# Performance work log

Hardware: AMD Instinct MI355X
Metric: run time of the kernel (lower is better)

## Reference

```python
import jax, jax.numpy as jnp
import numpy as np

S, N, A = 64, 4096, 32
HID, DM, NH, DK = 256, 128, 4, 32
EPS = 1e-5
SCALE = float(np.sqrt(DK))


def setup_inputs() -> dict:
    key = jax.random.key(0)
    ks = jax.random.split(key, 20)
    w = lambda i, sh: jax.random.normal(ks[i], sh, jnp.float32) * 0.02
    z = lambda n: jnp.zeros((n,), jnp.float32)
    return {
        "agent_states": jax.random.normal(ks[0], (N, S), jnp.float32),
        "sw1": w(1, (N * S, HID)), "sb1": z(HID),
        "sw2": w(2, (HID, HID)), "sb2": z(HID),
        "sow": w(3, (HID, 64)), "sob": z(64),
        "tw": w(4, (S + 64, DM)), "tb": z(DM),
        "wq": w(5, (DM, DM)), "bq": z(DM),
        "wk": w(6, (DM, DM)), "bk": z(DM),
        "wv": w(7, (DM, DM)), "bv": z(DM),
        "wo": w(8, (DM, DM)), "bo": z(DM),
        "ln_g": jnp.ones((DM,), jnp.float32), "ln_b": z(DM),
        "taw1": w(9, (DM, 64)), "tab1": z(64),
        "taw2": w(10, (64, 32)), "tab2": z(32),
        "ow1": w(11, (S + DM + 32, 256)), "ob1": z(256),
        "ow2": w(12, (256, DM)), "ob2": z(DM),
        "aw": w(13, (DM, A)), "ab": z(A),
        "vw": w(14, (DM, 1)), "vb": z(1),
        "cw": w(15, (S, 64)), "cb": z(64),
        "cdw": w(16, (64, 32)), "cdb": z(32),
    }


def reference(agent_states, sw1, sb1, sw2, sb2, sow, sob, tw, tb,
              wq, bq, wk, bk, wv, bv, wo, bo, ln_g, ln_b,
              taw1, tab1, taw2, tab2, ow1, ob1, ow2, ob2,
              aw, ab, vw, vb, cw, cb, cdw, cdb):
    n = agent_states.shape[0]
    # strategic level: flatten all agent states -> global objective [64]
    gs = agent_states.reshape(-1)
    strat = jax.nn.relu(jax.nn.relu(gs @ sw1 + sb1) @ sw2 + sb2)
    gobj = strat @ sow + sob
    # tactical encode (batched over agents instead of Python loop)
    tact_in = jnp.concatenate(
        [agent_states, jnp.broadcast_to(gobj, (n, gobj.shape[0]))], axis=-1)
    tact = jax.nn.relu(tact_in @ tw + tb)[None]  # [1, n, DM]
    # multi-head attention across agents
    q = (tact @ wq + bq).reshape(1, n, NH, DK).transpose(0, 2, 1, 3)
    k = (tact @ wk + bk).reshape(1, n, NH, DK).transpose(0, 2, 1, 3)
    v = (tact @ wv + bv).reshape(1, n, NH, DK).transpose(0, 2, 1, 3)
    scores = jnp.einsum('bhqd,bhkd->bhqk', q, k) / SCALE
    attn = jax.nn.softmax(scores, axis=-1)  # [1, NH, n, n]
    ctx = jnp.einsum('bhqk,bhkd->bhqd', attn, v).transpose(0, 2, 1, 3).reshape(1, n, DM)
    res = ctx @ wo + bo + tact
    mu = res.mean(-1, keepdims=True)
    var = res.var(-1, keepdims=True)  # biased, like torch LayerNorm
    coord = ((res - mu) / jnp.sqrt(var + EPS) * ln_g + ln_b)[0]  # [n, DM]
    # task allocation (softmax over 32 tasks)
    task = jax.nn.softmax(jax.nn.relu(coord @ taw1 + tab1) @ taw2 + tab2, axis=-1)
    # operational level -> actions / values
    op_in = jnp.concatenate([agent_states, coord, task], axis=-1)
    opf = jax.nn.relu(jax.nn.relu(op_in @ ow1 + ob1) @ ow2 + ob2)
    actions = opf @ aw + ab
    values = opf @ vw + vb
    # communication messages (two stacked linears, no activation in source)
    messages = (agent_states @ cw + cb) @ cdw + cdb
    return actions, values, messages, task, attn, gobj
```

## Files before the change

kernel.cpp:

```cpp
#include <hip/hip_runtime.h>

typedef __attribute__((ext_vector_type(8))) short s8v;
typedef __attribute__((ext_vector_type(4))) float f4v;

#define MFMA16(a, b, c) __builtin_amdgcn_mfma_f32_16x16x32_bf16((a), (b), (c), 0, 0, 0)

#define NAG   4096
#define SDIM  64
#define DMOD  128
#define NHD   4
#define DKD   32
#define HIDD  256
static constexpr float INV_SCALE = 0.17677669529663687f;
static constexpr float EPSV = 1e-5f;

#define OFF_ACT   0
#define OFF_VAL   131072
#define OFF_MSG   135168
#define OFF_TASK  266240
#define OFF_ATTN  397312
#define OFF_GOBJ  67506176

static constexpr size_t WS_P1   = 0;
static constexpr size_t WS_P1B  = 524288;
static constexpr size_t WS_P2   = 540672;
static constexpr size_t WS_TACT = 558080;
static constexpr size_t WS_Q    = 2655232;
static constexpr size_t WS_K    = 3703808;
static constexpr size_t WS_VT   = 4752384;
static constexpr size_t WS_CTX  = 5800960;
static constexpr size_t WS_OPIN = 7898112;
static constexpr size_t WS_H    = 9733120;
static constexpr size_t WS_OPF  = 11830272;
static constexpr size_t WS_OW1T = 12878848;
static constexpr size_t WS_OW2T = 12993536;

typedef unsigned short u16;
typedef unsigned int   u32;

static __device__ __forceinline__ u16 f2bf(float f) {
    union { float f; u32 u; } x; x.f = f;
    u32 r = x.u + 0x7FFFu + ((x.u >> 16) & 1u);
    return (u16)(r >> 16);
}
static __device__ __forceinline__ float bf2f(u16 b) {
    union { u32 u; float f; } x; x.u = ((u32)b) << 16;
    return x.f;
}

__global__ __launch_bounds__(256) void k1_sw1(const float* __restrict__ gs,
                                              const float* __restrict__ sw1,
                                              float* __restrict__ p1,
                                              const float* __restrict__ ow1,
                                              const float* __restrict__ ow2,
                                              u16* __restrict__ w1t,
                                              u16* __restrict__ w2t) {
    int tid = threadIdx.x;
    int b = blockIdx.x;
    if (b >= 512) {
        int bb = b - 512;
        if (bb < 224) {
            w1t[tid * 224 + bb] = f2bf(ow1[bb * 256 + tid]);
        } else if (tid < 128) {
            int k0 = (bb - 224) * 8;
#pragma unroll
            for (int kk = 0; kk < 8; ++kk) {
                int k = k0 + kk;
                w2t[tid * 256 + k] = f2bf(ow2[k * 128 + tid]);
            }
        }
        return;
    }
    __shared__ float gsl[512];
    __shared__ float red[4][256];
    gsl[tid]       = gs[b * 512 + tid];
    gsl[tid + 256] = gs[b * 512 + 256 + tid];
    __syncthreads();
    int t = tid & 63;
    int rg = tid >> 6;
    const f4v* w4 = (const f4v*)sw1;
    f4v acc = {0.f, 0.f, 0.f, 0.f};
    size_t rb = (size_t)b * 512;
#pragma unroll 4
    for (int r = rg; r < 512; r += 4) {
        float g = gsl[r];
        f4v w = __builtin_nontemporal_load(&w4[(rb + r) * 64 + t]);
        acc[0] += g * w[0]; acc[1] += g * w[1]; acc[2] += g * w[2]; acc[3] += g * w[3];
    }
    red[rg][4 * t + 0] = acc[0]; red[rg][4 * t + 1] = acc[1];
    red[rg][4 * t + 2] = acc[2]; red[rg][4 * t + 3] = acc[3];
    __syncthreads();
    float s = red[0][tid] + red[1][tid] + red[2][tid] + red[3][tid];
    p1[b * 256 + tid] = s;
}

__global__ void k1b_red(const float* __restrict__ p1, float* __restrict__ p1b) {
    int j = threadIdx.x;
    int b0 = blockIdx.x * 32;
    float s = 0.f;
#pragma unroll
    for (int b = 0; b < 32; ++b) s += p1[(b0 + b) * 256 + j];
    p1b[blockIdx.x * 256 + j] = s;
}

__global__ void k2b_strat(const float* __restrict__ p1b, const float* __restrict__ sb1,
                          const float* __restrict__ sw2, float* __restrict__ p2) {
    __shared__ float h1[256];
    int j = threadIdx.x;
    float s = 0.f;
#pragma unroll
    for (int b = 0; b < 16; ++b) s += p1b[b * 256 + j];
    h1[j] = fmaxf(s + sb1[j], 0.f);
    __syncthreads();
    int i0 = blockIdx.x * 16;
    float acc = 0.f;
#pragma unroll
    for (int i = 0; i < 16; ++i) acc += h1[i0 + i] * sw2[(i0 + i) * 256 + j];
    p2[blockIdx.x * 256 + j] = acc;
}

__global__ __launch_bounds__(256) void k3_tact_qkv(
    const float* __restrict__ p2, const float* __restrict__ sb2,
    const float* __restrict__ sow, const float* __restrict__ sob,
    const float* __restrict__ as, const float* __restrict__ tw, const float* __restrict__ tb,
    const float* __restrict__ wq, const float* __restrict__ bq,
    const float* __restrict__ wk, const float* __restrict__ bk,
    const float* __restrict__ wv, const float* __restrict__ bv,
    float* __restrict__ out_gobj, float* __restrict__ tactws,
    u16* __restrict__ qws, u16* __restrict__ kws, u16* __restrict__ vtws) {
    __shared__ float strat[256];
    __shared__ float gobj[64];
    __shared__ float asl[16][64];
    __shared__ float tl[16][128];
    int tid = threadIdx.x;
    int a0 = blockIdx.x * 16;
    {
        float s = 0.f;
#pragma unroll
        for (int b = 0; b < 16; ++b) s += p2[b * 256 + tid];
        strat[tid] = fmaxf(s + sb2[tid], 0.f);
    }
#pragma unroll
    for (int r = 0; r < 4; ++r) {
        int idx = tid + r * 256;
        asl[idx >> 6][idx & 63] = as[a0 * 64 + idx];
    }
    __syncthreads();
    if (tid < 64) {
        float g = sob[tid];
        for (int i = 0; i < 256; ++i) g += strat[i] * sow[i * 64 + tid];
        gobj[tid] = g;
        if (blockIdx.x == 0) out_gobj[tid] = g;
    }
    __syncthreads();
    int ah = tid >> 7, j = tid & 127;
    float gacc = 0.f;
    for (int i = 0; i < 64; ++i) gacc += gobj[i] * tw[(64 + i) * 128 + j];
    float acc[8];
    float base = tb[j] + gacc;
#pragma unroll
    for (int a = 0; a < 8; ++a) acc[a] = base;
    for (int i = 0; i < 64; ++i) {
        float w = tw[i * 128 + j];
#pragma unroll
        for (int a = 0; a < 8; ++a) acc[a] += asl[ah * 8 + a][i] * w;
    }
#pragma unroll
    for (int a = 0; a < 8; ++a) {
        float t = fmaxf(acc[a], 0.f);
        tl[ah * 8 + a][j] = t;
        tactws[(size_t)(a0 + ah * 8 + a) * 128 + j] = t;
    }
    __syncthreads();
    int h = j >> 5, d = j & 31;
#pragma unroll
    for (int a = 0; a < 8; ++a) acc[a] = 0.f;
    for (int i = 0; i < 128; ++i) {
        float w = wq[i * 128 + j];
#pragma unroll
        for (int a = 0; a < 8; ++a) acc[a] += tl[ah * 8 + a][i] * w;
    }
#pragma unroll
    for (int a = 0; a < 8; ++a)
        qws[h * 131072 + (a0 + ah * 8 + a) * 32 + d] = f2bf((acc[a] + bq[j]) * INV_SCALE);
#pragma unroll
    for (int a = 0; a < 8; ++a) acc[a] = 0.f;
    for (int i = 0; i < 128; ++i) {
        float w = wk[i * 128 + j];
#pragma unroll
        for (int a = 0; a < 8; ++a) acc[a] += tl[ah * 8 + a][i] * w;
    }
#pragma unroll
    for (int a = 0; a < 8; ++a)
        kws[h * 131072 + (a0 + ah * 8 + a) * 32 + d] = f2bf(acc[a] + bk[j]);
#pragma unroll
    for (int a = 0; a < 8; ++a) acc[a] = 0.f;
    for (int i = 0; i < 128; ++i) {
        float w = wv[i * 128 + j];
#pragma unroll
        for (int a = 0; a < 8; ++a) acc[a] += tl[ah * 8 + a][i] * w;
    }
    union { u16 u[8]; s8v v; } pk;
#pragma unroll
    for (int a = 0; a < 8; ++a) pk.u[a] = f2bf(acc[a] + bv[j]);
    *(s8v*)(vtws + h * 131072 + d * 4096 + a0 + ah * 8) = pk.v;
}

__global__ __launch_bounds__(512) void k4_attn(
    const u16* __restrict__ qws, const u16* __restrict__ kws, const u16* __restrict__ vtws,
    float* __restrict__ attn, float* __restrict__ ctxws) {
    int tid = threadIdx.x;
    int wid = tid >> 6;
    int l = tid & 63;
    int g = l >> 4;
    int ln = l & 15;
    int h = blockIdx.x >> 8;
    int qt = (blockIdx.x & 255) * 16;
    const u16* qh = qws + h * 131072;
    const u16* kh = kws + h * 131072;
    const u16* vh = vtws + h * 131072;
    int j0 = wid * 512;

    s8v aq = *(const s8v*)(qh + (qt + ln) * 32 + 8 * g);
    f4v zero = {0.f, 0.f, 0.f, 0.f};

    __shared__ __align__(16) union SmemU {
        struct {
            float red[8][16];
            u16 ldsPb[8][2][16][40];
            float pctx[8][16][32];
        } a;
        float sT[16][516];
    } sm;

    f4v lacc = zero, accA = zero, accB = zero;
    int buf = 0;
    for (int jc = 0; jc < 16; ++jc) {
        int jb = j0 + jc * 32;
        s8v b0 = *(const s8v*)(kh + (jb + ln) * 32 + 8 * g);
        s8v b1 = *(const s8v*)(kh + (jb + 16 + ln) * 32 + 8 * g);
        f4v S0 = MFMA16(aq, b0, zero);
        f4v S1 = MFMA16(aq, b1, zero);
#pragma unroll
        for (int r = 0; r < 4; ++r) {
            float w0 = __expf(S0[r]);
            float w1 = __expf(S1[r]);
            lacc[r] += w0 + w1;
            sm.a.ldsPb[wid][buf][4 * g + r][ln] = f2bf(w0);
            sm.a.ldsPb[wid][buf][4 * g + r][16 + ln] = f2bf(w1);
        }
        s8v bp = *(const s8v*)&sm.a.ldsPb[wid][buf][ln][8 * g];
        s8v va = *(const s8v*)(vh + ln * 4096 + jb + 8 * g);
        s8v vb = *(const s8v*)(vh + (16 + ln) * 4096 + jb + 8 * g);
        accA = MFMA16(va, bp, accA);
        accB = MFMA16(vb, bp, accB);
        buf ^= 1;
    }
#pragma unroll
    for (int m = 1; m <= 8; m <<= 1) {
        lacc[0] += __shfl_xor(lacc[0], m);
        lacc[1] += __shfl_xor(lacc[1], m);
        lacc[2] += __shfl_xor(lacc[2], m);
        lacc[3] += __shfl_xor(lacc[3], m);
    }
    if (ln == 0) {
#pragma unroll
        for (int r = 0; r < 4; ++r) sm.a.red[wid][4 * g + r] = lacc[r];
    }
    __syncthreads();
    float linvq = 1.f / (sm.a.red[0][ln] + sm.a.red[1][ln] + sm.a.red[2][ln] + sm.a.red[3][ln] +
                         sm.a.red[4][ln] + sm.a.red[5][ln] + sm.a.red[6][ln] + sm.a.red[7][ln]);
#pragma unroll
    for (int r = 0; r < 4; ++r) {
        sm.a.pctx[wid][ln][4 * g + r] = accA[r] * linvq;
        sm.a.pctx[wid][ln][16 + 4 * g + r] = accB[r] * linvq;
    }
    __syncthreads();
    {
        int q = tid >> 5;
        int d = tid & 31;
        float s = sm.a.pctx[0][q][d] + sm.a.pctx[1][q][d] + sm.a.pctx[2][q][d] + sm.a.pctx[3][q][d] +
                  sm.a.pctx[4][q][d] + sm.a.pctx[5][q][d] + sm.a.pctx[6][q][d] + sm.a.pctx[7][q][d];
        ctxws[(size_t)(qt + q) * 128 + h * 32 + d] = s;
    }
    __syncthreads();

    float* attnh = attn + (size_t)h * 4096 * 4096;
    for (int c = 0; c < 8; ++c) {
#pragma unroll
        for (int it = 0; it < 2; ++it) {
            int co = wid * 64 + it * 32;
            int jb = c * 512 + co;
            s8v b0 = *(const s8v*)(kh + (jb + ln) * 32 + 8 * g);
            s8v b1 = *(const s8v*)(kh + (jb + 16 + ln) * 32 + 8 * g);
            f4v S0 = MFMA16(b0, aq, zero);
            f4v S1 = MFMA16(b1, aq, zero);
            f4v o0, o1;
#pragma unroll
            for (int r = 0; r < 4; ++r) {
                o0[r] = __expf(S0[r]) * linvq;
                o1[r] = __expf(S1[r]) * linvq;
            }
            *(f4v*)&sm.sT[ln][co + 4 * g] = o0;
            *(f4v*)&sm.sT[ln][co + 16 + 4 * g] = o1;
        }
        __syncthreads();
#pragma unroll
        for (int r2 = 0; r2 < 2; ++r2) {
            int row = 2 * wid + r2;
            float* dst = attnh + (size_t)(qt + row) * 4096 + c * 512;
            f4v t0 = *(const f4v*)&sm.sT[row][4 * l];
            f4v t1 = *(const f4v*)&sm.sT[row][256 + 4 * l];
            *(f4v*)(dst + 4 * l) = t0;
            *(f4v*)(dst + 256 + 4 * l) = t1;
        }
        __syncthreads();
    }
}

__global__ __launch_bounds__(512) void k5_post(
    const float* __restrict__ ctxws, const float* __restrict__ tactws,
    const float* __restrict__ wo, const float* __restrict__ bo,
    const float* __restrict__ lng, const float* __restrict__ lnb,
    const float* __restrict__ taw1, const float* __restrict__ tab1,
    const float* __restrict__ taw2, const float* __restrict__ tab2,
    const float* __restrict__ as, float* __restrict__ dout, u16* __restrict__ opin) {
    __shared__ float wos[128 * 128];
    __shared__ float tw1s[128 * 64];
    __shared__ float tw2s[64 * 32];
    __shared__ float cx[8][128];
    __shared__ float coords[8][128];
    __shared__ float t1v[8][64];
    int tid = threadIdx.x;
    for (int i = tid; i < 128 * 128; i += 512) wos[i] = wo[i];
    for (int i = tid; i < 128 * 64; i += 512) tw1s[i] = taw1[i];
    for (int i = tid; i < 64 * 32; i += 512) tw2s[i] = taw2[i];
    __syncthreads();
    int w = tid >> 6, l = tid & 63;
    for (int it = 0; it < 2; ++it) {
        int n = blockIdx.x * 16 + w * 2 + it;
        float c0 = ctxws[(size_t)n * 128 + l], c1 = ctxws[(size_t)n * 128 + 64 + l];
        float t0 = tactws[(size_t)n * 128 + l], t1 = tactws[(size_t)n * 128 + 64 + l];
        float av = as[n * 64 + l];
        cx[w][l] = c0; cx[w][64 + l] = c1;
        __syncthreads();
        float r0 = bo[l] + t0, r1 = bo[64 + l] + t1;
        for (int k = 0; k < 128; ++k) {
            float cv = cx[w][k];
            r0 += cv * wos[k * 128 + l];
            r1 += cv * wos[k * 128 + 64 + l];
        }
        float s = r0 + r1;
#pragma unroll
        for (int m = 1; m <= 32; m <<= 1) s += __shfl_xor(s, m);
        float mu = s * (1.f / 128.f);
        float d0 = r0 - mu, d1 = r1 - mu;
        float vs = d0 * d0 + d1 * d1;
#pragma unroll
        for (int m = 1; m <= 32; m <<= 1) vs += __shfl_xor(vs, m);
        float rstd = 1.f / sqrtf(vs * (1.f / 128.f) + EPSV);
        float co0 = d0 * rstd * lng[l] + lnb[l];
        float co1 = d1 * rstd * lng[64 + l] + lnb[64 + l];
        coords[w][l] = co0; coords[w][64 + l] = co1;
        opin[(size_t)n * 224 + l] = f2bf(av);
        opin[(size_t)n * 224 + 64 + l] = f2bf(co0);
        opin[(size_t)n * 224 + 128 + l] = f2bf(co1);
        __syncthreads();
        float a1 = tab1[l];
        for (int i = 0; i < 128; ++i) a1 += coords[w][i] * tw1s[i * 64 + l];
        t1v[w][l] = fmaxf(a1, 0.f);
        __syncthreads();
        if (l < 32) {
            float a2 = tab2[l];
            for (int i = 0; i < 64; ++i) a2 += t1v[w][i] * tw2s[i * 32 + l];
            float mx = a2;
#pragma unroll
            for (int m = 1; m <= 16; m <<= 1) mx = fmaxf(mx, __shfl_xor(mx, m));
            float e = __expf(a2 - mx);
            float se = e;
#pragma unroll
            for (int m = 1; m <= 16; m <<= 1) se += __shfl_xor(se, m);
            float tk = e / se;
            dout[OFF_TASK + n * 32 + l] = tk;
            opin[(size_t)n * 224 + 192 + l] = f2bf(tk);
        }
        __syncthreads();
    }
}

__global__ __launch_bounds__(256) void k6a(const u16* __restrict__ opin, const u16* __restrict__ w1t,
                                           const float* __restrict__ ob1, u16* __restrict__ Hws) {
    int tid = threadIdx.x;
    int w = tid >> 6, l = tid & 63, g = l >> 4, ln = l & 15;
    int bm = blockIdx.x & 63, bn = blockIdx.x >> 6;
    int m0 = bm * 64 + w * 16, n0 = bn * 64;
    f4v acc[4];
    f4v zero = {0.f, 0.f, 0.f, 0.f};
#pragma unroll
    for (int nt = 0; nt < 4; ++nt) acc[nt] = zero;
    for (int kt = 0; kt < 7; ++kt) {
        s8v A = *(const s8v*)(opin + (size_t)(m0 + ln) * 224 + kt * 32 + 8 * g);
#pragma unroll
        for (int nt = 0; nt < 4; ++nt) {
            s8v B = *(const s8v*)(w1t + (size_t)(n0 + nt * 16 + ln) * 224 + kt * 32 + 8 * g);
            acc[nt] = MFMA16(A, B, acc[nt]);
        }
    }
#pragma unroll
    for (int nt = 0; nt < 4; ++nt) {
        int col = n0 + nt * 16 + ln;
        float bias = ob1[col];
#pragma unroll
        for (int r = 0; r < 4; ++r) {
            int row = m0 + 4 * g + r;
            Hws[(size_t)row * 256 + col] = f2bf(fmaxf(acc[nt][r] + bias, 0.f));
        }
    }
}

__global__ __launch_bounds__(256) void k6b(const u16* __restrict__ Hws, const u16* __restrict__ w2t,
                                           const float* __restrict__ ob2, u16* __restrict__ opfws) {
    int tid = threadIdx.x;
    int w = tid >> 6, l = tid & 63, g = l >> 4, ln = l & 15;
    int bm = blockIdx.x & 63, bn = blockIdx.x >> 6;
    int m0 = bm * 64 + w * 16, n0 = bn * 64;
    f4v acc[4];
    f4v zero = {0.f, 0.f, 0.f, 0.f};
#pragma unroll
    for (int nt = 0; nt < 4; ++nt) acc[nt] = zero;
    for (int kt = 0; kt < 8; ++kt) {
        s8v A = *(const s8v*)(Hws + (size_t)(m0 + ln) * 256 + kt * 32 + 8 * g);
#pragma unroll
        for (int nt = 0; nt < 4; ++nt) {
            s8v B = *(const s8v*)(w2t + (size_t)(n0 + nt * 16 + ln) * 256 + kt * 32 + 8 * g);
            acc[nt] = MFMA16(A, B, acc[nt]);
        }
    }
#pragma unroll
    for (int nt = 0; nt < 4; ++nt) {
        int col = n0 + nt * 16 + ln;
        float bias = ob2[col];
#pragma unroll
        for (int r = 0; r < 4; ++r) {
            int row = m0 + 4 * g + r;
            opfws[(size_t)row * 128 + col] = f2bf(fmaxf(acc[nt][r] + bias, 0.f));
        }
    }
}

__global__ __launch_bounds__(256) void k6c(const u16* __restrict__ opf, const float* __restrict__ as,
                                           const float* __restrict__ aw, const float* __restrict__ ab,
                                           const float* __restrict__ vw, const float* __restrict__ vb,
                                           const float* __restrict__ cw, const float* __restrict__ cb,
                                           const float* __restrict__ cdw, const float* __restrict__ cdb,
                                           float* __restrict__ dout) {
    __shared__ float opfs[4][128];
    __shared__ float asl[4][64];
    __shared__ float m1s[4][64];
    int tid = threadIdx.x;
    int w = tid >> 6, l = tid & 63;
    int n = blockIdx.x * 4 + w;
    {
        u32 u = *(const u32*)(opf + (size_t)n * 128 + 2 * l);
        opfs[w][2 * l] = bf2f((u16)(u & 0xffff));
        opfs[w][2 * l + 1] = bf2f((u16)(u >> 16));
        asl[w][l] = as[n * 64 + l];
    }
    __syncthreads();
    if (l < 32) {
        float a = ab[l];
        for (int k = 0; k < 128; ++k) a += opfs[w][k] * aw[k * 32 + l];
        dout[OFF_ACT + n * 32 + l] = a;
    }
    {
        float p = opfs[w][l] * vw[l] + opfs[w][64 + l] * vw[64 + l];
#pragma unroll
        for (int m = 1; m <= 32; m <<= 1) p += __shfl_xor(p, m);
        if (l == 0) dout[OFF_VAL + n] = p + vb[0];
    }
    {
        float a = cb[l];
        for (int k = 0; k < 64; ++k) a += asl[w][k] * cw[k * 64 + l];
        m1s[w][l] = a;
    }
    __syncthreads();
    if (l < 32) {
        float a = cdb[l];
        for (int k = 0; k < 64; ++k) a += m1s[w][k] * cdw[k * 32 + l];
        dout[OFF_MSG + n * 32 + l] = a;
    }
}

extern "C" void kernel_launch(void* const* d_in, const int* in_sizes, int n_in,
                              void* d_out, int out_size, void* d_ws, size_t ws_size,
                              hipStream_t stream) {
    const float* as  = (const float*)d_in[0];
    const float* sw1 = (const float*)d_in[1];
    const float* sb1 = (const float*)d_in[2];
    const float* sw2 = (const float*)d_in[3];
    const float* sb2 = (const float*)d_in[4];
    const float* sow = (const float*)d_in[5];
    const float* sob = (const float*)d_in[6];
    const float* tw  = (const float*)d_in[7];
    const float* tb  = (const float*)d_in[8];
    const float* wq  = (const float*)d_in[9];
    const float* bq  = (const float*)d_in[10];
    const float* wk  = (const float*)d_in[11];
    const float* bk  = (const float*)d_in[12];
    const float* wv  = (const float*)d_in[13];
    const float* bv  = (const float*)d_in[14];
    const float* wo  = (const float*)d_in[15];
    const float* bo  = (const float*)d_in[16];
    const float* lng = (const float*)d_in[17];
    const float* lnb = (const float*)d_in[18];
    const float* taw1 = (const float*)d_in[19];
    const float* tab1 = (const float*)d_in[20];
    const float* taw2 = (const float*)d_in[21];
    const float* tab2 = (const float*)d_in[22];
    const float* ow1 = (const float*)d_in[23];
    const float* ob1 = (const float*)d_in[24];
    const float* ow2 = (const float*)d_in[25];
    const float* ob2 = (const float*)d_in[26];
    const float* aw  = (const float*)d_in[27];
    const float* ab  = (const float*)d_in[28];
    const float* vw  = (const float*)d_in[29];
    const float* vb  = (const float*)d_in[30];
    const float* cw  = (const float*)d_in[31];
    const float* cb  = (const float*)d_in[32];
    const float* cdw = (const float*)d_in[33];
    const float* cdb = (const float*)d_in[34];

    float* dout = (float*)d_out;
    char* ws = (char*)d_ws;
    float* p1    = (float*)(ws + WS_P1);
    float* p1b   = (float*)(ws + WS_P1B);
    float* p2    = (float*)(ws + WS_P2);
    float* tactw = (float*)(ws + WS_TACT);
    u16*   qws   = (u16*)(ws + WS_Q);
    u16*   kws   = (u16*)(ws + WS_K);
    u16*   vtws  = (u16*)(ws + WS_VT);
    float* ctxws = (float*)(ws + WS_CTX);
    u16*   opin  = (u16*)(ws + WS_OPIN);
    u16*   Hws   = (u16*)(ws + WS_H);
    u16*   opfws = (u16*)(ws + WS_OPF);
    u16*   w1t   = (u16*)(ws + WS_OW1T);
    u16*   w2t   = (u16*)(ws + WS_OW2T);

    hipLaunchKernelGGL(k1_sw1, dim3(768), dim3(256), 0, stream, as, sw1, p1, ow1, ow2, w1t, w2t);
    hipLaunchKernelGGL(k1b_red, dim3(16), dim3(256), 0, stream, p1, p1b);
    hipLaunchKernelGGL(k2b_strat, dim3(16), dim3(256), 0, stream, p1b, sb1, sw2, p2);
    hipLaunchKernelGGL(k3_tact_qkv, dim3(256), dim3(256), 0, stream,
                       p2, sb2, sow, sob, as, tw, tb, wq, bq, wk, bk, wv, bv,
                       dout + OFF_GOBJ, tactw, qws, kws, vtws);
    hipLaunchKernelGGL(k4_attn, dim3(1024), dim3(512), 0, stream,
                       qws, kws, vtws, dout + OFF_ATTN, ctxws);
    hipLaunchKernelGGL(k5_post, dim3(256), dim3(512), 0, stream,
                       ctxws, tactw, wo, bo, lng, lnb, taw1, tab1, taw2, tab2, as, dout, opin);
    hipLaunchKernelGGL(k6a, dim3(256), dim3(256), 0, stream, opin, w1t, ob1, Hws);
    hipLaunchKernelGGL(k6b, dim3(128), dim3(256), 0, stream, Hws, w2t, ob2, opfws);
    hipLaunchKernelGGL(k6c, dim3(1024), dim3(256), 0, stream,
                       opfws, as, aw, ab, vw, vb, cw, cb, cdw, cdb, dout);
}
```

Baseline: 209.6 us.

## Double-buffer attention-matrix write-out and halve agents per block in QKV kernel

The attention probability write-out loop in k4_attn now works on 256-column chunks held in two alternating LDS buffers. The global store of chunk c-1 is interleaved with computing chunk c, which leaves one barrier per iteration instead of two. Separately, k3_tact_qkv processes 8 agents per block instead of 16 and launches 512 blocks, so the small per-agent projection work is spread over more CUs. The trade-off is more iterations and smaller store bursts in k4, and more redundant gobj/strat recomputation across the doubled k3 blocks.

Measured after the change: 194.5 us. -7.2%, faster.

```diff
diff --git a/kernel.cpp b/kernel.cpp
--- a/kernel.cpp
+++ b/kernel.cpp
@@ -1,6 +1,7 @@
 #include <hip/hip_runtime.h>
 
 typedef __attribute__((ext_vector_type(8))) short s8v;
+typedef __attribute__((ext_vector_type(4))) short s4v;
 typedef __attribute__((ext_vector_type(4))) float f4v;
 
 #define MFMA16(a, b, c) __builtin_amdgcn_mfma_f32_16x16x32_bf16((a), (b), (c), 0, 0, 0)
@@ -130,10 +131,10 @@
     u16* __restrict__ qws, u16* __restrict__ kws, u16* __restrict__ vtws) {
     __shared__ float strat[256];
     __shared__ float gobj[64];
-    __shared__ float asl[16][64];
-    __shared__ float tl[16][128];
-    int tid = threadIdx.x;
-    int a0 = blockIdx.x * 16;
+    __shared__ float asl[8][64];
+    __shared__ float tl[8][128];
+    int tid = threadIdx.x;
+    int a0 = blockIdx.x * 8;
     {
         float s = 0.f;
 #pragma unroll
@@ -141,7 +142,7 @@
         strat[tid] = fmaxf(s + sb2[tid], 0.f);
     }
 #pragma unroll
-    for (int r = 0; r < 4; ++r) {
+    for (int r = 0; r < 2; ++r) {
         int idx = tid + r * 256;
         asl[idx >> 6][idx & 63] = as[a0 * 64 + idx];
     }
@@ -156,54 +157,54 @@
     int ah = tid >> 7, j = tid & 127;
     float gacc = 0.f;
     for (int i = 0; i < 64; ++i) gacc += gobj[i] * tw[(64 + i) * 128 + j];
-    float acc[8];
+    float acc[4];
     float base = tb[j] + gacc;
 #pragma unroll
-    for (int a = 0; a < 8; ++a) acc[a] = base;
+    for (int a = 0; a < 4; ++a) acc[a] = base;
     for (int i = 0; i < 64; ++i) {
         float w = tw[i * 128 + j];
 #pragma unroll
-        for (int a = 0; a < 8; ++a) acc[a] += asl[ah * 8 + a][i] * w;
-    }
-#pragma unroll
-    for (int a = 0; a < 8; ++a) {
+        for (int a = 0; a < 4; ++a) acc[a] += asl[ah * 4 + a][i] * w;
+    }
+#pragma unroll
+    for (int a = 0; a < 4; ++a) {
         float t = fmaxf(acc[a], 0.f);
-        tl[ah * 8 + a][j] = t;
-        tactws[(size_t)(a0 + ah * 8 + a) * 128 + j] = t;
+        tl[ah * 4 + a][j] = t;
+        tactws[(size_t)(a0 + ah * 4 + a) * 128 + j] = t;
     }
     __syncthreads();
     int h = j >> 5, d = j & 31;
 #pragma unroll
-    for (int a = 0; a < 8; ++a) acc[a] = 0.f;
+    for (int a = 0; a < 4; ++a) acc[a] = 0.f;
     for (int i = 0; i < 128; ++i) {
         float w = wq[i * 128 + j];
 #pragma unroll
-        for (int a = 0; a < 8; ++a) acc[a] += tl[ah * 8 + a][i] * w;
-    }
-#pragma unroll
-    for (int a = 0; a < 8; ++a)
-        qws[h * 131072 + (a0 + ah * 8 + a) * 32 + d] = f2bf((acc[a] + bq[j]) * INV_SCALE);
-#pragma unroll
-    for (int a = 0; a < 8; ++a) acc[a] = 0.f;
+        for (int a = 0; a < 4; ++a) acc[a] += tl[ah * 4 + a][i] * w;
+    }
+#pragma unroll
+    for (int a = 0; a < 4; ++a)
+        qws[h * 131072 + (a0 + ah * 4 + a) * 32 + d] = f2bf((acc[a] + bq[j]) * INV_SCALE);
+#pragma unroll
+    for (int a = 0; a < 4; ++a) acc[a] = 0.f;
     for (int i = 0; i < 128; ++i) {
         float w = wk[i * 128 + j];
 #pragma unroll
-        for (int a = 0; a < 8; ++a) acc[a] += tl[ah * 8 + a][i] * w;
-    }
-#pragma unroll
-    for (int a = 0; a < 8; ++a)
-        kws[h * 131072 + (a0 + ah * 8 + a) * 32 + d] = f2bf(acc[a] + bk[j]);
-#pragma unroll
-    for (int a = 0; a < 8; ++a) acc[a] = 0.f;
+        for (int a = 0; a < 4; ++a) acc[a] += tl[ah * 4 + a][i] * w;
+    }
+#pragma unroll
+    for (int a = 0; a < 4; ++a)
+        kws[h * 131072 + (a0 + ah * 4 + a) * 32 + d] = f2bf(acc[a] + bk[j]);
+#pragma unroll
+    for (int a = 0; a < 4; ++a) acc[a] = 0.f;
     for (int i = 0; i < 128; ++i) {
         float w = wv[i * 128 + j];
 #pragma unroll
-        for (int a = 0; a < 8; ++a) acc[a] += tl[ah * 8 + a][i] * w;
-    }
-    union { u16 u[8]; s8v v; } pk;
-#pragma unroll
-    for (int a = 0; a < 8; ++a) pk.u[a] = f2bf(acc[a] + bv[j]);
-    *(s8v*)(vtws + h * 131072 + d * 4096 + a0 + ah * 8) = pk.v;
+        for (int a = 0; a < 4; ++a) acc[a] += tl[ah * 4 + a][i] * w;
+    }
+    union { u16 u[4]; s4v v; } pk;
+#pragma unroll
+    for (int a = 0; a < 4; ++a) pk.u[a] = f2bf(acc[a] + bv[j]);
+    *(s4v*)(vtws + h * 131072 + d * 4096 + a0 + ah * 4) = pk.v;
 }
 
 __global__ __launch_bounds__(512) void k4_attn(
@@ -230,7 +231,7 @@
             u16 ldsPb[8][2][16][40];
             float pctx[8][16][32];
         } a;
-        float sT[16][516];
+        float sT[2][16][260];
     } sm;
 
     f4v lacc = zero, accA = zero, accB = zero;
@@ -286,36 +287,38 @@
     __syncthreads();
 
     float* attnh = attn + (size_t)h * 4096 * 4096;
-    for (int c = 0; c < 8; ++c) {
-#pragma unroll
-        for (int it = 0; it < 2; ++it) {
-            int co = wid * 64 + it * 32;
-            int jb = c * 512 + co;
-            s8v b0 = *(const s8v*)(kh + (jb + ln) * 32 + 8 * g);
-            s8v b1 = *(const s8v*)(kh + (jb + 16 + ln) * 32 + 8 * g);
-            f4v S0 = MFMA16(b0, aq, zero);
-            f4v S1 = MFMA16(b1, aq, zero);
-            f4v o0, o1;
-#pragma unroll
-            for (int r = 0; r < 4; ++r) {
-                o0[r] = __expf(S0[r]) * linvq;
-                o1[r] = __expf(S1[r]) * linvq;
-            }
-            *(f4v*)&sm.sT[ln][co + 4 * g] = o0;
-            *(f4v*)&sm.sT[ln][co + 16 + 4 * g] = o1;
-        }
-        __syncthreads();
+    auto COMPUTE = [&](int c, int p) {
+        int co = wid * 32;
+        int jb = c * 256 + co;
+        s8v b0 = *(const s8v*)(kh + (jb + ln) * 32 + 8 * g);
+        s8v b1 = *(const s8v*)(kh + (jb + 16 + ln) * 32 + 8 * g);
+        f4v S0 = MFMA16(b0, aq, zero);
+        f4v S1 = MFMA16(b1, aq, zero);
+        f4v o0, o1;
+#pragma unroll
+        for (int r = 0; r < 4; ++r) {
+            o0[r] = __expf(S0[r]) * linvq;
+            o1[r] = __expf(S1[r]) * linvq;
+        }
+        *(f4v*)&sm.sT[p][ln][co + 4 * g] = o0;
+        *(f4v*)&sm.sT[p][ln][co + 16 + 4 * g] = o1;
+    };
+    auto STORE = [&](int c, int p) {
 #pragma unroll
         for (int r2 = 0; r2 < 2; ++r2) {
             int row = 2 * wid + r2;
-            float* dst = attnh + (size_t)(qt + row) * 4096 + c * 512;
-            f4v t0 = *(const f4v*)&sm.sT[row][4 * l];
-            f4v t1 = *(const f4v*)&sm.sT[row][256 + 4 * l];
-            *(f4v*)(dst + 4 * l) = t0;
-            *(f4v*)(dst + 256 + 4 * l) = t1;
-        }
+            f4v t = *(const f4v*)&sm.sT[p][row][4 * l];
+            *(f4v*)(attnh + (size_t)(qt + row) * 4096 + c * 256 + 4 * l) = t;
+        }
+    };
+    COMPUTE(0, 0);
+    __syncthreads();
+    for (int c = 1; c < 16; ++c) {
+        STORE(c - 1, (c - 1) & 1);
+        COMPUTE(c, c & 1);
         __syncthreads();
     }
+    STORE(15, 1);
 }
 
 __global__ __launch_bounds__(512) void k5_post(
@@ -549,7 +552,7 @@
     hipLaunchKernelGGL(k1_sw1, dim3(768), dim3(256), 0, stream, as, sw1, p1, ow1, ow2, w1t, w2t);
     hipLaunchKernelGGL(k1b_red, dim3(16), dim3(256), 0, stream, p1, p1b);
     hipLaunchKernelGGL(k2b_strat, dim3(16), dim3(256), 0, stream, p1b, sb1, sw2, p2);
-    hipLaunchKernelGGL(k3_tact_qkv, dim3(256), dim3(256), 0, stream,
+    hipLaunchKernelGGL(k3_tact_qkv, dim3(512), dim3(256), 0, stream,
                        p2, sb2, sow, sob, as, tw, tb, wq, bq, wk, bk, wv, bv,
                        dout + OFF_GOBJ, tactw, qws, kws, vtws);
     hipLaunchKernelGGL(k4_attn, dim3(1024), dim3(512), 0, stream,
```
